# Optimization experiments

Hardware: AMD Instinct MI355X
Metric: run time of the kernel (lower is better)

## Reference

```python
import jax, jax.numpy as jnp
import numpy as np

B, S, D, H = 2, 2048, 1024, 16
DH = D // H  # per-head attention dim


def setup_inputs() -> dict:
    key = jax.random.key(0)
    ks = jax.random.split(key, 11)
    scale = 0.02
    return {
        "query": jax.random.normal(ks[0], (B, S, D), jnp.float32),
        "key": jax.random.normal(ks[1], (B, S, D), jnp.float32),
        "value": jax.random.normal(ks[2], (B, S, D), jnp.float32),
        # per-head QKV projection weights, stacked over heads: [H, D, DH]
        "Wq": jax.random.normal(ks[3], (H, D, DH), jnp.float32) * scale,
        "bq": jnp.zeros((H, DH), jnp.float32),
        "Wk": jax.random.normal(ks[4], (H, D, DH), jnp.float32) * scale,
        "bk": jnp.zeros((H, DH), jnp.float32),
        "Wv": jax.random.normal(ks[5], (H, D, DH), jnp.float32) * scale,
        "bv": jnp.zeros((H, DH), jnp.float32),
        # output linear: [D, D]
        "Wo": jax.random.normal(ks[6], (D, D), jnp.float32) * scale,
        "bo": jnp.zeros((D,), jnp.float32),
        "look_ahead_mask": 1,
    }


def reference(query, key, value, Wq, bq, Wk, bk, Wv, bv, Wo, bo, look_ahead_mask):
    # batched per-head projections: [B,S,D] x [H,D,E] -> [B,H,S,E]
    q = jnp.einsum("bsd,hde->bhse", query, Wq) + bq[None, :, None, :]
    k = jnp.einsum("bsd,hde->bhse", key, Wk) + bk[None, :, None, :]
    v = jnp.einsum("bsd,hde->bhse", value, Wv) + bv[None, :, None, :]
    scores = jnp.einsum("bhqe,bhke->bhqk", q, k) / jnp.sqrt(jnp.float32(DH))
    if look_ahead_mask:
        causal = jnp.tril(jnp.ones((S, S), bool))
        scores = jnp.where(causal[None, None], scores, jnp.float32(-1e9))
    probs = jax.nn.softmax(scores, axis=-1)
    ctx = jnp.einsum("bhqk,bhke->bhqe", probs, v)  # [B,H,S,DH]
    # concat heads along last dim (head order matches ModuleList order)
    concat = ctx.transpose(0, 2, 1, 3).reshape(B, S, D)
    return concat @ Wo + bo
```

## Files before the change

### kernel.cpp

```cpp
#include <hip/hip_runtime.h>


typedef short bf16x8 __attribute__((ext_vector_type(8)));
typedef float f32x4 __attribute__((ext_vector_type(4)));

__device__ __forceinline__ unsigned short f2bf(float f){
  unsigned int u = __builtin_bit_cast(unsigned int, f);
  u = (u + 0x7fffu + ((u >> 16) & 1u)) >> 16;
  return (unsigned short)u;
}

__device__ __forceinline__ void gld_lds16(const void* src, void* dst){
  __builtin_amdgcn_global_load_lds((const __attribute__((address_space(1))) unsigned int*)src,
                                   (__attribute__((address_space(3))) unsigned int*)dst,
                                   16, 0, 0);
}

__device__ __forceinline__ void stage_lds(const char* gtile, size_t growb, char* lds,
                                          int tid, int rowb_lg2, int swz, int tilebytes){
  int w = tid >> 6;
  for (int c = 0; c < tilebytes; c += 4096){
    int o = c + tid*16;
    int row = o >> rowb_lg2;
    int colb = o & ((1 << rowb_lg2) - 1);
    if (swz) colb ^= ((row & 7) << 4);
    gld_lds16(gtile + (size_t)row*growb + colb, lds + c + w*1024);
  }
}

__global__ __launch_bounds__(256) void convert3(const float* __restrict__ a,
                                                const float* __restrict__ b,
                                                const float* __restrict__ c,
                                                unsigned short* __restrict__ outa,
                                                unsigned short* __restrict__ outb,
                                                unsigned short* __restrict__ outc){
  int i = blockIdx.x*blockDim.x + threadIdx.x;
  int seg = i >> 19, il = i & 524287;
  const float* in = seg==0 ? a : (seg==1 ? b : c);
  unsigned short* out = seg==0 ? outa : (seg==1 ? outb : outc);
  const float4* p = (const float4*)in;
  float4 x = p[2*il], y = p[2*il+1];
  uint4 o;
  o.x = (unsigned int)f2bf(x.x) | ((unsigned int)f2bf(x.y) << 16);
  o.y = (unsigned int)f2bf(x.z) | ((unsigned int)f2bf(x.w) << 16);
  o.z = (unsigned int)f2bf(y.x) | ((unsigned int)f2bf(y.y) << 16);
  o.w = (unsigned int)f2bf(y.z) | ((unsigned int)f2bf(y.w) << 16);
  ((uint4*)out)[il] = o;
}

__global__ __launch_bounds__(256) void transpose_bf16(const float* __restrict__ in,
                                                      unsigned short* __restrict__ out,
                                                      int R, int C,
                                                      size_t in_mstride, size_t out_mstride){
  __shared__ unsigned short tile[64][66];
  int t = threadIdx.x;
  int r0 = blockIdx.x*64, c0 = blockIdx.y*64;
  const float* inm = in + (size_t)blockIdx.z*in_mstride;
  unsigned short* outm = out + (size_t)blockIdx.z*out_mstride;
  int j = t & 63, i0 = (t >> 6)*16;
  #pragma unroll
  for (int ii = 0; ii < 16; ii++){
    int i = i0 + ii;
    tile[i][j] = f2bf(inm[(size_t)(r0+i)*C + c0 + j]);
  }
  __syncthreads();
  #pragma unroll
  for (int ii = 0; ii < 16; ii++){
    int i = i0 + ii;
    outm[(size_t)(c0+i)*R + r0 + j] = tile[j][i];
  }
}

template<int EPI>
__device__ __forceinline__ void gemm_body(const unsigned short* A, const unsigned short* BT,
                                          const float* bias, void* outp, float scale,
                                          unsigned short (*lA)[128*32], unsigned short (*lB)[128*32]){
  const int K = 1024, N = 1024;
  int tid = threadIdx.x, lane = tid & 63, w = tid >> 6;
  int bn = blockIdx.x*128, bm = blockIdx.y*128;
  int wm = (w >> 1)*64, wn = (w & 1)*64;
  int lr = lane & 15;
  int lkb = (lane >> 4)*16;
  const char* Ab = (const char*)(A + (size_t)bm*K);
  const char* Bb = (const char*)(BT + (size_t)bn*K);
  size_t grow = (size_t)K*2;
  int nk = K >> 5;

  f32x4 zf = {0.f,0.f,0.f,0.f};
  f32x4 acc[4][4];
  #pragma unroll
  for (int mi = 0; mi < 4; mi++)
    #pragma unroll
    for (int ni = 0; ni < 4; ni++) acc[mi][ni] = zf;

  stage_lds(Ab, grow, (char*)lA[0], tid, 6, 0, 8192);
  stage_lds(Bb, grow, (char*)lB[0], tid, 6, 0, 8192);
  __syncthreads();
  int cur = 0;
  for (int kt = 0; kt < nk; kt++){
    if (kt + 1 < nk){
      stage_lds(Ab + (size_t)(kt+1)*64, grow, (char*)lA[cur^1], tid, 6, 0, 8192);
      stage_lds(Bb + (size_t)(kt+1)*64, grow, (char*)lB[cur^1], tid, 6, 0, 8192);
    }
    const char* pa = (const char*)lA[cur];
    const char* pb = (const char*)lB[cur];
    bf16x8 af[4], bfr[4];
    #pragma unroll
    for (int mi = 0; mi < 4; mi++)
      af[mi] = *(const bf16x8*)(pa + (wm + mi*16 + lr)*64 + lkb);
    #pragma unroll
    for (int ni = 0; ni < 4; ni++)
      bfr[ni] = *(const bf16x8*)(pb + (wn + ni*16 + lr)*64 + lkb);
    #pragma unroll
    for (int mi = 0; mi < 4; mi++)
      #pragma unroll
      for (int ni = 0; ni < 4; ni++)
        acc[mi][ni] = __builtin_amdgcn_mfma_f32_16x16x32_bf16(af[mi], bfr[ni], acc[mi][ni], 0, 0, 0);
    __syncthreads();
    cur ^= 1;
  }

  #pragma unroll
  for (int mi = 0; mi < 4; mi++)
    #pragma unroll
    for (int ni = 0; ni < 4; ni++)
      #pragma unroll
      for (int r = 0; r < 4; r++){
        int row = bm + wm + mi*16 + (lane >> 4)*4 + r;
        int col = bn + wn + ni*16 + (lane & 15);
        float v = acc[mi][ni][r] + bias[col];
        if (EPI == 0){
          v *= scale;
          unsigned short* o = (unsigned short*)outp;
          o[(size_t)((row >> 11)*16 + (col >> 6))*131072 + (size_t)(row & 2047)*64 + (col & 63)] = f2bf(v);
        } else {
          float* o = (float*)outp;
          o[(size_t)row*N + col] = v;
        }
      }
}

__global__ __launch_bounds__(256) void gemm_qkv(const unsigned short* __restrict__ Xq,
                                                const unsigned short* __restrict__ Xk,
                                                const unsigned short* __restrict__ Xv,
                                                const unsigned short* __restrict__ WqT,
                                                const unsigned short* __restrict__ WkT,
                                                const unsigned short* __restrict__ WvT,
                                                const float* __restrict__ bq,
                                                const float* __restrict__ bk,
                                                const float* __restrict__ bv,
                                                unsigned short* __restrict__ oq,
                                                unsigned short* __restrict__ ok,
                                                unsigned short* __restrict__ ov){
  __shared__ __align__(16) unsigned short lA[2][128*32];
  __shared__ __align__(16) unsigned short lB[2][128*32];
  int z = blockIdx.z;
  const unsigned short* A  = z==0 ? Xq  : (z==1 ? Xk  : Xv);
  const unsigned short* BT = z==0 ? WqT : (z==1 ? WkT : WvT);
  const float* bias        = z==0 ? bq  : (z==1 ? bk  : bv);
  unsigned short* out      = z==0 ? oq  : (z==1 ? ok  : ov);
  float scale = z==0 ? 0.125f : 1.0f;
  gemm_body<0>(A, BT, bias, out, scale, lA, lB);
}

__global__ __launch_bounds__(256) void gemm_out(const unsigned short* __restrict__ A,
                                                const unsigned short* __restrict__ BT,
                                                const float* __restrict__ bias,
                                                float* __restrict__ outp){
  __shared__ __align__(16) unsigned short lA[2][128*32];
  __shared__ __align__(16) unsigned short lB[2][128*32];
  gemm_body<1>(A, BT, bias, outp, 1.0f, lA, lB);
}

__global__ __launch_bounds__(256) void attn_fwd(const unsigned short* __restrict__ qh,
                                                const unsigned short* __restrict__ kh,
                                                const unsigned short* __restrict__ vh,
                                                unsigned short* __restrict__ cc,
                                                const int* __restrict__ maskp){
  __shared__ __align__(16) unsigned short Qs[64*64];
  __shared__ __align__(16) unsigned short Ks[64*64];
  __shared__ __align__(16) unsigned short VTs[64*64];
  __shared__ __align__(16) unsigned short Ps[4][16*64];
  int tid = threadIdx.x, lane = tid & 63, w = tid >> 6;
  int lg = lane >> 4, lr = lane & 15;
  int qt = blockIdx.x, bh = blockIdx.y;
  size_t base = (size_t)bh * (2048*64);
  const unsigned short* Q = qh + base;
  const unsigned short* K = kh + base;
  const unsigned short* V = vh + base;
  int q0 = qt*64;
  int causal = *maskp;

  stage_lds((const char*)(Q + (size_t)q0*64), 128, (char*)Qs, tid, 7, 1, 8192);
  __syncthreads();

  bf16x8 qf[2];
  #pragma unroll
  for (int kk = 0; kk < 2; kk++){
    int row = w*16 + lr;
    qf[kk] = *(const bf16x8*)((const char*)Qs + row*128 + ((kk*64 + lg*16) ^ ((row & 7) << 4)));
  }

  f32x4 zf = {0.f,0.f,0.f,0.f};
  f32x4 oa[4];
  float mr[4], lsm[4];
  #pragma unroll
  for (int ei = 0; ei < 4; ei++) oa[ei] = zf;
  #pragma unroll
  for (int r = 0; r < 4; r++){ mr[r] = -1e30f; lsm[r] = 0.f; }

  int nt = causal ? (qt + 1) : 32;
  int wq0 = q0 + w*16;

  for (int t = 0; t < nt; t++){
    __syncthreads();
    stage_lds((const char*)(K + (size_t)t*4096), 128, (char*)Ks, tid, 7, 1, 8192);
    #pragma unroll
    for (int c = 0; c < 2; c++){
      int o = c*4096 + tid*16;
      uint4 vvv = *(const uint4*)((const char*)V + (size_t)t*8192 + o);
      int kv = o >> 7;
      int e0 = (o & 127) >> 1;
      unsigned int uu[4] = {vvv.x, vvv.y, vvv.z, vvv.w};
      #pragma unroll
      for (int j = 0; j < 4; j++){
        int e1 = e0 + 2*j, e2 = e1 + 1;
        *(unsigned short*)((char*)VTs + e1*128 + ((kv*2) ^ ((e1 & 7) << 4))) = (unsigned short)(uu[j] & 0xffffu);
        *(unsigned short*)((char*)VTs + e2*128 + ((kv*2) ^ ((e2 & 7) << 4))) = (unsigned short)(uu[j] >> 16);
      }
    }
    __syncthreads();

    if (causal && (t*64 > wq0 + 15)) continue;

    f32x4 sc[4];
    #pragma unroll
    for (int ni = 0; ni < 4; ni++) sc[ni] = zf;
    #pragma unroll
    for (int kk = 0; kk < 2; kk++)
      #pragma unroll
      for (int ni = 0; ni < 4; ni++){
        int krow = ni*16 + lr;
        bf16x8 kf = *(const bf16x8*)((const char*)Ks + krow*128 + ((kk*64 + lg*16) ^ ((krow & 7) << 4)));
        sc[ni] = __builtin_amdgcn_mfma_f32_16x16x32_bf16(qf[kk], kf, sc[ni], 0, 0, 0);
      }

    if (causal && (t*64 + 63 > wq0)){
      #pragma unroll
      for (int ni = 0; ni < 4; ni++)
        #pragma unroll
        for (int r = 0; r < 4; r++){
          int qrow = wq0 + lg*4 + r;
          int kvc  = t*64 + ni*16 + lr;
          if (kvc > qrow) sc[ni][r] = -1e9f;
        }
    }

    #pragma unroll
    for (int r = 0; r < 4; r++){
      float mx = fmaxf(fmaxf(sc[0][r], sc[1][r]), fmaxf(sc[2][r], sc[3][r]));
      #pragma unroll
      for (int off = 1; off < 16; off <<= 1)
        mx = fmaxf(mx, __shfl_xor(mx, off, 64));
      float mo = mr[r];
      float mn = fmaxf(mo, mx);
      mr[r] = mn;
      float alpha = __expf(mo - mn);
      float psum = 0.f;
      #pragma unroll
      for (int ni = 0; ni < 4; ni++){
        float p = __expf(sc[ni][r] - mn);
        sc[ni][r] = p;
        psum += p;
      }
      #pragma unroll
      for (int off = 1; off < 16; off <<= 1)
        psum += __shfl_xor(psum, off, 64);
      lsm[r] = lsm[r]*alpha + psum;
      #pragma unroll
      for (int ei = 0; ei < 4; ei++) oa[ei][r] *= alpha;
    }

    #pragma unroll
    for (int ni = 0; ni < 4; ni++)
      #pragma unroll
      for (int r = 0; r < 4; r++){
        int prow = lg*4 + r;
        int pcb = (ni*16 + lr)*2;
        *(unsigned short*)((char*)Ps[w] + prow*128 + (pcb ^ ((prow & 7) << 4))) = f2bf(sc[ni][r]);
      }

    #pragma unroll
    for (int kk = 0; kk < 2; kk++){
      bf16x8 pf = *(const bf16x8*)((const char*)Ps[w] + lr*128 + ((kk*64 + lg*16) ^ ((lr & 7) << 4)));
      #pragma unroll
      for (int ei = 0; ei < 4; ei++){
        int vrow = ei*16 + lr;
        bf16x8 vf = *(const bf16x8*)((const char*)VTs + vrow*128 + ((kk*64 + lg*16) ^ ((vrow & 7) << 4)));
        oa[ei] = __builtin_amdgcn_mfma_f32_16x16x32_bf16(pf, vf, oa[ei], 0, 0, 0);
      }
    }
  }

  int b = bh >> 4, h = bh & 15;
  #pragma unroll
  for (int r = 0; r < 4; r++){
    float inv = 1.f / lsm[r];
    int q = q0 + w*16 + lg*4 + r;
    size_t rowbase = (size_t)(b*2048 + q)*1024 + h*64;
    #pragma unroll
    for (int ei = 0; ei < 4; ei++){
      int e = ei*16 + lr;
      cc[rowbase + e] = f2bf(oa[ei][r] * inv);
    }
  }
}

extern "C" void kernel_launch(void* const* d_in, const int* in_sizes, int n_in,
                              void* d_out, int out_size, void* d_ws, size_t ws_size,
                              hipStream_t stream){
  const float* query = (const float*)d_in[0];
  const float* key_i = (const float*)d_in[1];
  const float* value = (const float*)d_in[2];
  const float* Wq = (const float*)d_in[3];
  const float* bq = (const float*)d_in[4];
  const float* Wk = (const float*)d_in[5];
  const float* bk = (const float*)d_in[6];
  const float* Wv = (const float*)d_in[7];
  const float* bv = (const float*)d_in[8];
  const float* Wo = (const float*)d_in[9];
  const float* bo = (const float*)d_in[10];
  const int* mask = (const int*)d_in[11];

  char* ws = (char*)d_ws;
  const size_t ACT = 8388608;
  unsigned short* Xq  = (unsigned short*)(ws + 0*ACT);
  unsigned short* Xk  = (unsigned short*)(ws + 1*ACT);
  unsigned short* Xv  = (unsigned short*)(ws + 2*ACT);
  unsigned short* qh  = (unsigned short*)(ws + 3*ACT);
  unsigned short* kh  = (unsigned short*)(ws + 4*ACT);
  unsigned short* vh  = (unsigned short*)(ws + 5*ACT);
  unsigned short* cc  = (unsigned short*)(ws + 6*ACT);
  unsigned short* WqT = (unsigned short*)(ws + 7*ACT);
  unsigned short* WkT = (unsigned short*)(ws + 7*ACT + 2097152);
  unsigned short* WvT = (unsigned short*)(ws + 7*ACT + 4194304);
  unsigned short* WoT = (unsigned short*)(ws + 7*ACT + 6291456);

  convert3<<<6144, 256, 0, stream>>>(query, key_i, value, Xq, Xk, Xv);

  transpose_bf16<<<dim3(16,1,16), 256, 0, stream>>>(Wq, WqT, 1024, 64, 65536, 65536);
  transpose_bf16<<<dim3(16,1,16), 256, 0, stream>>>(Wk, WkT, 1024, 64, 65536, 65536);
  transpose_bf16<<<dim3(16,1,16), 256, 0, stream>>>(Wv, WvT, 1024, 64, 65536, 65536);
  transpose_bf16<<<dim3(16,16,1), 256, 0, stream>>>(Wo, WoT, 1024, 1024, 0, 0);

  gemm_qkv<<<dim3(8,32,3), 256, 0, stream>>>(Xq, Xk, Xv, WqT, WkT, WvT, bq, bk, bv, qh, kh, vh);

  attn_fwd<<<dim3(32,32), 256, 0, stream>>>(qh, kh, vh, cc, mask);

  gemm_out<<<dim3(8,32), 256, 0, stream>>>(cc, WoT, bo, (float*)d_out);
}
```

Measured before the change: 359.3 us.

## Pre-transpose V globally and stream K/V from global memory in attention

Adds a separate kernel that transposes V once per head into a workspace buffer, and rewrites attention so each wave reads Q, K and V^T fragments straight from global memory instead of staging them in LDS behind block barriers. Query tiles are issued heaviest-first by reversing the block index so long causal tiles start early. This removes per-tile LDS staging, the scalar LDS transpose of V and the __syncthreads, at the cost of an extra kernel launch, extra global traffic and uncoalesced strided loads that depend on L2 reuse across waves.

```diff
diff --git a/kernel.cpp b/kernel.cpp
--- a/kernel.cpp
+++ b/kernel.cpp
@@ -68,6 +68,27 @@
   for (int ii = 0; ii < 16; ii++){
     int i = i0 + ii;
     outm[(size_t)(c0+i)*R + r0 + j] = tile[j][i];
+  }
+}
+
+__global__ __launch_bounds__(256) void transpose_v(const unsigned short* __restrict__ in,
+                                                   unsigned short* __restrict__ out){
+  __shared__ unsigned short tile[64][66];
+  int t = threadIdx.x;
+  int s0 = blockIdx.x*64;
+  const unsigned short* inm = in + (size_t)blockIdx.y*131072;
+  unsigned short* outm = out + (size_t)blockIdx.y*131072;
+  int j = t & 63, i0 = (t >> 6)*16;
+  #pragma unroll
+  for (int ii = 0; ii < 16; ii++){
+    int i = i0 + ii;
+    tile[i][j] = inm[(size_t)(s0+i)*64 + j];
+  }
+  __syncthreads();
+  #pragma unroll
+  for (int ii = 0; ii < 16; ii++){
+    int i = i0 + ii;
+    outm[(size_t)i*2048 + s0 + j] = tile[j][i];
   }
 }
 
@@ -172,34 +193,28 @@
   gemm_body<1>(A, BT, bias, outp, 1.0f, lA, lB);
 }
 
-__global__ __launch_bounds__(256) void attn_fwd(const unsigned short* __restrict__ qh,
-                                                const unsigned short* __restrict__ kh,
-                                                const unsigned short* __restrict__ vh,
-                                                unsigned short* __restrict__ cc,
-                                                const int* __restrict__ maskp){
-  __shared__ __align__(16) unsigned short Qs[64*64];
-  __shared__ __align__(16) unsigned short Ks[64*64];
-  __shared__ __align__(16) unsigned short VTs[64*64];
+__global__ __launch_bounds__(256) void attn_fwd2(const unsigned short* __restrict__ qh,
+                                                 const unsigned short* __restrict__ kh,
+                                                 const unsigned short* __restrict__ vt,
+                                                 unsigned short* __restrict__ cc,
+                                                 const int* __restrict__ maskp){
   __shared__ __align__(16) unsigned short Ps[4][16*64];
   int tid = threadIdx.x, lane = tid & 63, w = tid >> 6;
   int lg = lane >> 4, lr = lane & 15;
-  int qt = blockIdx.x, bh = blockIdx.y;
-  size_t base = (size_t)bh * (2048*64);
-  const unsigned short* Q = qh + base;
-  const unsigned short* K = kh + base;
-  const unsigned short* V = vh + base;
-  int q0 = qt*64;
+  int bid = blockIdx.x;
+  int bh = bid & 31;
+  int qquad = 31 - (bid >> 5);
   int causal = *maskp;
-
-  stage_lds((const char*)(Q + (size_t)q0*64), 128, (char*)Qs, tid, 7, 1, 8192);
-  __syncthreads();
+  int g = qquad*4 + w;
+  int wq0 = g*16;
+  const char* Q  = (const char*)(qh + (size_t)bh*131072);
+  const char* K  = (const char*)(kh + (size_t)bh*131072);
+  const char* VT = (const char*)(vt + (size_t)bh*131072);
 
   bf16x8 qf[2];
   #pragma unroll
-  for (int kk = 0; kk < 2; kk++){
-    int row = w*16 + lr;
-    qf[kk] = *(const bf16x8*)((const char*)Qs + row*128 + ((kk*64 + lg*16) ^ ((row & 7) << 4)));
-  }
+  for (int kk = 0; kk < 2; kk++)
+    qf[kk] = *(const bf16x8*)(Q + (size_t)(wq0 + lr)*128 + kk*64 + lg*16);
 
   f32x4 zf = {0.f,0.f,0.f,0.f};
   f32x4 oa[4];
@@ -209,29 +224,15 @@
   #pragma unroll
   for (int r = 0; r < 4; r++){ mr[r] = -1e30f; lsm[r] = 0.f; }
 
-  int nt = causal ? (qt + 1) : 32;
-  int wq0 = q0 + w*16;
+  int nt = causal ? (qquad + 1) : 32;
 
   for (int t = 0; t < nt; t++){
-    __syncthreads();
-    stage_lds((const char*)(K + (size_t)t*4096), 128, (char*)Ks, tid, 7, 1, 8192);
-    #pragma unroll
-    for (int c = 0; c < 2; c++){
-      int o = c*4096 + tid*16;
-      uint4 vvv = *(const uint4*)((const char*)V + (size_t)t*8192 + o);
-      int kv = o >> 7;
-      int e0 = (o & 127) >> 1;
-      unsigned int uu[4] = {vvv.x, vvv.y, vvv.z, vvv.w};
-      #pragma unroll
-      for (int j = 0; j < 4; j++){
-        int e1 = e0 + 2*j, e2 = e1 + 1;
-        *(unsigned short*)((char*)VTs + e1*128 + ((kv*2) ^ ((e1 & 7) << 4))) = (unsigned short)(uu[j] & 0xffffu);
-        *(unsigned short*)((char*)VTs + e2*128 + ((kv*2) ^ ((e2 & 7) << 4))) = (unsigned short)(uu[j] >> 16);
-      }
-    }
-    __syncthreads();
-
-    if (causal && (t*64 > wq0 + 15)) continue;
+    bf16x8 kf[2][4];
+    #pragma unroll
+    for (int kk = 0; kk < 2; kk++)
+      #pragma unroll
+      for (int ni = 0; ni < 4; ni++)
+        kf[kk][ni] = *(const bf16x8*)(K + (size_t)(t*64 + ni*16 + lr)*128 + kk*64 + lg*16);
 
     f32x4 sc[4];
     #pragma unroll
@@ -239,11 +240,8 @@
     #pragma unroll
     for (int kk = 0; kk < 2; kk++)
       #pragma unroll
-      for (int ni = 0; ni < 4; ni++){
-        int krow = ni*16 + lr;
-        bf16x8 kf = *(const bf16x8*)((const char*)Ks + krow*128 + ((kk*64 + lg*16) ^ ((krow & 7) << 4)));
-        sc[ni] = __builtin_amdgcn_mfma_f32_16x16x32_bf16(qf[kk], kf, sc[ni], 0, 0, 0);
-      }
+      for (int ni = 0; ni < 4; ni++)
+        sc[ni] = __builtin_amdgcn_mfma_f32_16x16x32_bf16(qf[kk], kf[kk][ni], sc[ni], 0, 0, 0);
 
     if (causal && (t*64 + 63 > wq0)){
       #pragma unroll
@@ -295,8 +293,7 @@
       bf16x8 pf = *(const bf16x8*)((const char*)Ps[w] + lr*128 + ((kk*64 + lg*16) ^ ((lr & 7) << 4)));
       #pragma unroll
       for (int ei = 0; ei < 4; ei++){
-        int vrow = ei*16 + lr;
-        bf16x8 vf = *(const bf16x8*)((const char*)VTs + vrow*128 + ((kk*64 + lg*16) ^ ((vrow & 7) << 4)));
+        bf16x8 vf = *(const bf16x8*)(VT + (size_t)(ei*16 + lr)*4096 + t*128 + kk*64 + lg*16);
         oa[ei] = __builtin_amdgcn_mfma_f32_16x16x32_bf16(pf, vf, oa[ei], 0, 0, 0);
       }
     }
@@ -306,7 +303,7 @@
   #pragma unroll
   for (int r = 0; r < 4; r++){
     float inv = 1.f / lsm[r];
-    int q = q0 + w*16 + lg*4 + r;
+    int q = wq0 + lg*4 + r;
     size_t rowbase = (size_t)(b*2048 + q)*1024 + h*64;
     #pragma unroll
     for (int ei = 0; ei < 4; ei++){
@@ -345,6 +342,7 @@
   unsigned short* WkT = (unsigned short*)(ws + 7*ACT + 2097152);
   unsigned short* WvT = (unsigned short*)(ws + 7*ACT + 4194304);
   unsigned short* WoT = (unsigned short*)(ws + 7*ACT + 6291456);
+  unsigned short* vtr = Xq;
 
   convert3<<<6144, 256, 0, stream>>>(query, key_i, value, Xq, Xk, Xv);
 
@@ -355,7 +353,9 @@
 
   gemm_qkv<<<dim3(8,32,3), 256, 0, stream>>>(Xq, Xk, Xv, WqT, WkT, WvT, bq, bk, bv, qh, kh, vh);
 
-  attn_fwd<<<dim3(32,32), 256, 0, stream>>>(qh, kh, vh, cc, mask);
+  transpose_v<<<dim3(32,32), 256, 0, stream>>>(vh, vtr);
+
+  attn_fwd2<<<1024, 256, 0, stream>>>(qh, kh, vtr, cc, mask);
 
   gemm_out<<<dim3(8,32), 256, 0, stream>>>(cc, WoT, bo, (float*)d_out);
 }
```

Measured after the change: 336.7 us. -6.3%, faster.
